# Performance work log

Measured on AMD Instinct MI355X. Metric: run time of the kernel, lower is better.

Reference implementation:

```python
import jax, jax.numpy as jnp
import numpy as np

EPS = 1e-8
TAU = 1.0


def _spatial_adjacency(segments, n_seg):
    # segments: (B, H, W) int. Counts 4-neighbour pixel adjacencies between segments;
    # diagonal counts pixels per segment (self loops kept).
    B, H, W = segments.shape
    b = jnp.arange(B)[:, None]
    adj = jnp.zeros((B, n_seg, n_seg), jnp.float32)
    flat = segments.reshape(B, -1)
    adj = adj.at[b, flat, flat].add(1.0)  # self loops = segment sizes
    s1 = segments[:, :, :-1].reshape(B, -1)
    s2 = segments[:, :, 1:].reshape(B, -1)
    adj = adj.at[b, s1, s2].add(1.0).at[b, s2, s1].add(1.0)
    v1 = segments[:, :-1, :].reshape(B, -1)
    v2 = segments[:, 1:, :].reshape(B, -1)
    adj = adj.at[b, v1, v2].add(1.0).at[b, v2, v1].add(1.0)
    return adj


def _proximity_adjacency(segments, n_seg):
    adj = _spatial_adjacency(segments, n_seg)
    # zero connections of node 0 except its diagonal
    adj = adj.at[:, 1:, 0].set(0.0).at[:, 0, 1:].set(0.0)
    size_node = jnp.diagonal(adj, axis1=-2, axis2=-1)
    new_diag = adj.sum(axis=2) - size_node + 1.0
    idx = jnp.arange(n_seg)
    adj = adj.at[:, idx, idx].set(new_diag)
    # normalize_adjacency(binarize=True, normalize=False)
    return (adj > 0).astype(jnp.float32)


def setup_inputs() -> dict:
    key = jax.random.key(0)
    k1, k2, k3 = jax.random.split(key, 3)
    B, N, D, R = 8, 2048, 384, 64
    H = W = 256
    x = jax.random.normal(k1, (B, N, D), jnp.float32)
    segments = jax.random.randint(k2, (B, H, W), 0, N, jnp.int64)
    prototypes = jax.random.normal(k3, (1, R, D), jnp.float32)
    return {"x": x, "segments": segments, "prototypes": prototypes}


def reference(x, segments, prototypes):
    B, N, D = x.shape
    prox_adj = _proximity_adjacency(segments, N)  # (B, N, N) binary

    # node-presence mask (B, N)
    b = jnp.arange(B)[:, None]
    flat = segments.reshape(B, -1)
    mask = jnp.zeros((B, N), jnp.float32).at[b, flat].max(1.0)

    # cosine prototype clustering (Q = V = K = Identity)
    protos = prototypes[0]  # (R, D)
    qn = x / jnp.maximum(jnp.linalg.norm(x, axis=-1, keepdims=True), EPS)
    kn = protos / jnp.maximum(jnp.linalg.norm(protos, axis=-1, keepdims=True), EPS)
    Csim = (jnp.einsum('bnd,rd->bnr', qn, kn) + 1.0) * 0.5
    S = Csim / Csim.sum(axis=-1, keepdims=True)  # soft assignment (B, N, R)

    # cluster alignment loss (DEC-style sharpened-target KL, masked over present nodes)
    P = S ** 2 / (S.sum(axis=1, keepdims=True) + EPS)
    P = P / (P.sum(axis=-1, keepdims=True) + EPS)
    kl = (P * (jnp.log(P + EPS) - jnp.log(S + EPS))).sum(axis=-1)  # (B, N)
    loss = (kl * mask).sum() / (mask.sum() + EPS)

    # affinity adjacency from assignments
    C = jax.nn.softmax(S * TAU, axis=-1)  # (B, N, R)
    cn = jnp.linalg.norm(C, axis=-1)  # (B, N)
    proto_adj = jnp.einsum('bnr,bmr->bnm', C, C) / (cn[:, :, None] * cn[:, None, :] + EPS)
    adj = prox_adj * proto_adj
    # normalize_adjacency(normalize=True): row normalization
    adj = adj / (adj.sum(axis=-1, keepdims=True) + EPS)

    out = jnp.einsum('bnm,bmd->bnd', adj, x)  # adj @ values
    return out, segments, loss, C
```

## Files before the change

kernel.cpp:

```cpp
#include <hip/hip_runtime.h>
#include <hip/hip_bf16.h>

#define NB 8
#define NN 2048
#define ND 384
#define NR 64
#define OUT_ELEMS (NB*NN*ND)
#define SEG_ELEMS (NB*256*256)
#define NBLK_LOSS (NB*NN/4)

typedef float  f32x4  __attribute__((ext_vector_type(4)));
typedef short  bf16x8 __attribute__((ext_vector_type(8)));

__device__ inline float wsum(float v){
  #pragma unroll
  for(int o=32;o;o>>=1) v += __shfl_xor(v,o,64);
  return v;
}
__device__ inline float wmax(float v){
  #pragma unroll
  for(int o=32;o;o>>=1) v = fmaxf(v,__shfl_xor(v,o,64));
  return v;
}
__device__ inline unsigned short f2bf(float f){
  unsigned u = __float_as_uint(f);
  return (unsigned short)((u + 0x8000u) >> 16);
}

__device__ __forceinline__ void gl2lds16(const unsigned short* g, unsigned short* s){
  __builtin_amdgcn_global_load_lds(
      (const __attribute__((address_space(1))) unsigned int*)g,
      (__attribute__((address_space(3))) unsigned int*)s,
      16, 0, 0);
}

__global__ void k_proto(const float* __restrict__ protos, float* __restrict__ kn){
  int r = blockIdx.x, l = threadIdx.x;
  float v[6]; float ss = 0.f;
  #pragma unroll
  for(int i=0;i<6;i++){ v[i] = protos[r*ND + l*6 + i]; ss += v[i]*v[i]; }
  ss = wsum(ss);
  float inv = 1.f / fmaxf(sqrtf(ss), 1e-8f);
  #pragma unroll
  for(int i=0;i<6;i++) kn[r*ND + l*6 + i] = v[i]*inv;
}

__global__ __launch_bounds__(1024) void k_seg(const int* __restrict__ seg,
                                              float* __restrict__ mask,
                                              unsigned* __restrict__ prox){
  __shared__ unsigned lm[64*64];
  int tid = threadIdx.x;
  int b  = blockIdx.x & 7;
  int rg = blockIdx.x >> 3;
  int base = rg << 6;
  for(int i=tid; i<64*64; i+=1024) lm[i] = 0u;
  __syncthreads();
  const int* sb = seg + b*65536;

#define PAIR(S, S2) { \
    if((S) != (S2) && (S) != 0 && (S2) != 0){ \
      if(((S )>>6)==rg) atomicOr(&lm[(((S )&63)<<6) + ((S2)>>5)], 1u<<((S2)&31)); \
      if(((S2)>>6)==rg) atomicOr(&lm[(((S2)&63)<<6) + ((S )>>5)], 1u<<((S )&31)); \
    } }

  #pragma unroll 1
  for(int it=0; it<16; ++it){
    int g = it*1024 + tid;
    int p = g*4;
    int i = g >> 6;
    int j = (g & 63)*4;
    int4 a = *(const int4*)(sb + p);
    if((a.x>>6)==rg) mask[(b<<11) + a.x] = 1.f;
    if((a.y>>6)==rg) mask[(b<<11) + a.y] = 1.f;
    if((a.z>>6)==rg) mask[(b<<11) + a.z] = 1.f;
    if((a.w>>6)==rg) mask[(b<<11) + a.w] = 1.f;
    PAIR(a.x, a.y); PAIR(a.y, a.z); PAIR(a.z, a.w);
    if(j < 252){
      int n = sb[p + 4];
      PAIR(a.w, n);
    }
    if(i < 255){
      int4 v = *(const int4*)(sb + p + 256);
      PAIR(a.x, v.x); PAIR(a.y, v.y); PAIR(a.z, v.z); PAIR(a.w, v.w);
    }
  }
#undef PAIR
  __syncthreads();
  unsigned* dst = prox + ((size_t)(b<<11) + base)*64;
  *(uint4*)(dst + tid*4) = *(const uint4*)&lm[tid*4];
}

__global__ __launch_bounds__(256) void k_csim(const float* __restrict__ x,
                                              const float* __restrict__ kn,
                                              float* __restrict__ Sout,
                                              unsigned short* __restrict__ xTbf,
                                              float* __restrict__ part){
  __shared__ float xT[32*68];
  __shared__ float kT[32*68];
  __shared__ float xinvS[64];
  __shared__ float csh[16*64];
  int t = threadIdx.x;
  int m0 = blockIdx.x * 64;
  float acc[4][4] = {};
  int mload = t>>2, koff = (t&3)*8;
  int mb = (t>>4)*4, rb = (t&15)*4;
  float ssq = 0.f;
  for(int c=0;c<12;c++){
    int k0 = c*32;
    __syncthreads();
    const float4* xg = (const float4*)(x + (size_t)(m0+mload)*ND + k0 + koff);
    float4 a = xg[0], bq = xg[1];
    ssq += a.x*a.x + a.y*a.y + a.z*a.z + a.w*a.w
         + bq.x*bq.x + bq.y*bq.y + bq.z*bq.z + bq.w*bq.w;
    xT[(koff+0)*68+mload]=a.x;  xT[(koff+1)*68+mload]=a.y;  xT[(koff+2)*68+mload]=a.z;  xT[(koff+3)*68+mload]=a.w;
    xT[(koff+4)*68+mload]=bq.x; xT[(koff+5)*68+mload]=bq.y; xT[(koff+6)*68+mload]=bq.z; xT[(koff+7)*68+mload]=bq.w;
    const float4* kg = (const float4*)(kn + mload*ND + k0 + koff);
    float4 ka = kg[0], kb = kg[1];
    kT[(koff+0)*68+mload]=ka.x; kT[(koff+1)*68+mload]=ka.y; kT[(koff+2)*68+mload]=ka.z; kT[(koff+3)*68+mload]=ka.w;
    kT[(koff+4)*68+mload]=kb.x; kT[(koff+5)*68+mload]=kb.y; kT[(koff+6)*68+mload]=kb.z; kT[(koff+7)*68+mload]=kb.w;
    __syncthreads();
    {
      int k2 = t>>3, mo = (t&7)*8;
      const float* src = &xT[k2*68 + mo];
      float4 aa = *(const float4*)src;
      float4 bb = *(const float4*)(src+4);
      uint4 o;
      o.x = (unsigned)f2bf(aa.x) | ((unsigned)f2bf(aa.y)<<16);
      o.y = (unsigned)f2bf(aa.z) | ((unsigned)f2bf(aa.w)<<16);
      o.z = (unsigned)f2bf(bb.x) | ((unsigned)f2bf(bb.y)<<16);
      o.w = (unsigned)f2bf(bb.z) | ((unsigned)f2bf(bb.w)<<16);
      int bb2 = m0 >> 11, ml = m0 & 2047;
      *(uint4*)(xTbf + ((size_t)(bb2*ND + k0 + k2))*NN + ml + mo) = o;
    }
    for(int k=0;k<32;k++){
      float xv[4], kv[4];
      *(float4*)xv = *(const float4*)&xT[k*68+mb];
      *(float4*)kv = *(const float4*)&kT[k*68+rb];
      #pragma unroll
      for(int mi=0;mi<4;mi++)
        #pragma unroll
        for(int ri=0;ri<4;ri++) acc[mi][ri] += xv[mi]*kv[ri];
    }
  }
  ssq += __shfl_xor(ssq,1,64);
  ssq += __shfl_xor(ssq,2,64);
  if((t&3)==0) xinvS[mload] = 1.f / fmaxf(sqrtf(ssq), 1e-8f);
  __syncthreads();
  float sv[4][4];
  #pragma unroll
  for(int mi=0;mi<4;mi++){
    float xin = xinvS[mb+mi];
    float rsum = 0.f;
    #pragma unroll
    for(int ri=0;ri<4;ri++){
      float vv = (acc[mi][ri]*xin + 1.f)*0.5f;
      sv[mi][ri] = vv; rsum += vv;
    }
    rsum += __shfl_xor(rsum,1,64);
    rsum += __shfl_xor(rsum,2,64);
    rsum += __shfl_xor(rsum,4,64);
    rsum += __shfl_xor(rsum,8,64);
    float inv = 1.f/rsum;
    #pragma unroll
    for(int ri=0;ri<4;ri++) sv[mi][ri] *= inv;
    *(float4*)&Sout[(size_t)(m0+mb+mi)*NR + rb] = *(const float4*)sv[mi];
  }
  {
    float4 pc;
    pc.x = sv[0][0]+sv[1][0]+sv[2][0]+sv[3][0];
    pc.y = sv[0][1]+sv[1][1]+sv[2][1]+sv[3][1];
    pc.z = sv[0][2]+sv[1][2]+sv[2][2]+sv[3][2];
    pc.w = sv[0][3]+sv[1][3]+sv[2][3]+sv[3][3];
    *(float4*)&csh[(t>>4)*64 + rb] = pc;
  }
  __syncthreads();
  if(t < 64){
    float a = 0.f;
    #pragma unroll
    for(int g=0;g<16;g++) a += csh[g*64 + t];
    part[(size_t)blockIdx.x*64 + t] = a;
  }
}

__global__ void k_lossfc(float* Smat, const float* __restrict__ part,
                         const float* __restrict__ mask,
                         float* __restrict__ klp, float* __restrict__ mp,
                         unsigned short* __restrict__ Kbf){
  __shared__ float shk[4], shm[4];
  int w = threadIdx.x>>6, l = threadIdx.x&63;
  int node = blockIdx.x*4 + w;
  int b = node >> 11;
  float s = Smat[(size_t)node*NR + l];
  float csm = 0.f;
  #pragma unroll
  for(int c=0;c<32;c++) csm += part[(size_t)((b<<5)+c)*64 + l];
  float p = s*s/(csm + 1e-8f);
  float ps = wsum(p);
  float P = p/(ps + 1e-8f);
  float term = P*(logf(P + 1e-8f) - logf(s + 1e-8f));
  float kl = wsum(term);
  if(l==0){ float mv = mask[node]; shk[w] = kl*mv; shm[w] = mv; }
  float mx = wmax(s);
  float e = expf(s - mx);
  float Z = wsum(e);
  float c = e / Z;
  float cn2 = wsum(c*c);
  Smat[(size_t)node*NR + l] = c;
  Kbf[(size_t)node*NR + l] = f2bf(c * rsqrtf(cn2));
  __syncthreads();
  if(threadIdx.x==0){
    klp[blockIdx.x] = shk[0]+shk[1]+shk[2]+shk[3];
    mp [blockIdx.x] = shm[0]+shm[1]+shm[2]+shm[3];
  }
}

__global__ __launch_bounds__(256) void k_qk(const unsigned short* __restrict__ Kbf,
                                            const unsigned* __restrict__ prox,
                                            unsigned short* __restrict__ Pbf){
  __shared__ short Plds[64*72];
  int tid = threadIdx.x;
  int w = tid>>6, l = tid&63, q = l>>4, li = l&15;
  int b  = blockIdx.x & 7;
  int qt = (blockIdx.x>>3) & 31;
  int kt = blockIdx.x >> 8;
  const unsigned short* Kb = Kbf + (size_t)b*NN*NR;

  int arow = qt*64 + w*16 + li;
  bf16x8 af[2];
  af[0] = *(const bf16x8*)(Kb + (size_t)arow*NR + q*8);
  af[1] = *(const bf16x8*)(Kb + (size_t)arow*NR + 32 + q*8);
  f32x4 pacc[4] = {(f32x4)(0.f),(f32x4)(0.f),(f32x4)(0.f),(f32x4)(0.f)};
  #pragma unroll
  for(int f=0;f<4;f++){
    int brow = kt*64 + f*16 + li;
    bf16x8 b0 = *(const bf16x8*)(Kb + (size_t)brow*NR + q*8);
    bf16x8 b1 = *(const bf16x8*)(Kb + (size_t)brow*NR + 32 + q*8);
    pacc[f] = __builtin_amdgcn_mfma_f32_16x16x32_bf16(af[0], b0, pacc[f], 0,0,0);
    pacc[f] = __builtin_amdgcn_mfma_f32_16x16x32_bf16(af[1], b1, pacc[f], 0,0,0);
  }
  #pragma unroll
  for(int r=0;r<4;r++){
    int lrow = w*16 + q*4 + r;
    int grow = qt*64 + lrow;
    uint2 mw = *(const uint2*)(prox + ((size_t)(b*NN + grow))*64 + kt*2);
    if(qt==kt){
      if((lrow>>5)==0) mw.x |= 1u<<(lrow&31); else mw.y |= 1u<<(lrow&31);
    }
    #pragma unroll
    for(int f=0;f<4;f++){
      unsigned wd = (f<2) ? mw.x : mw.y;
      float v = ((wd >> ((f&1)*16 + li)) & 1u) ? pacc[f][r] : 0.f;
      Plds[lrow*72 + f*16 + li] = (short)f2bf(v);
    }
  }
  __syncthreads();
  {
    int row = tid>>2, sg = tid&3;
    const uint4* src = (const uint4*)&Plds[row*72 + sg*16];
    unsigned short* dst = Pbf + ((size_t)(b*NN + qt*64 + row))*NN + kt*64 + sg*16;
    uint4 v0 = src[0], v1 = *(const uint4*)((const short*)src + 8);
    *(uint4*)dst = v0;
    *(uint4*)(dst + 8) = v1;
  }
}

__global__ __launch_bounds__(256, 3) void k_pv(const unsigned short* __restrict__ Pbf,
                                               const unsigned short* __restrict__ xTbf,
                                               float* __restrict__ out){
  __shared__ unsigned short Al[64*32];
  __shared__ unsigned short Bl[128*32];
  int tid = threadIdx.x;
  int w = tid>>6, l = tid&63, q = l>>4, li = l&15;
  int b  = blockIdx.x & 7;
  int mt = (blockIdx.x>>3) & 31;
  int ct = blockIdx.x >> 8;
  int m0 = mt*64;
  int d0 = ct*128;
  const unsigned short* Pb  = Pbf  + (size_t)b*NN*NN;
  const unsigned short* xTb = xTbf + (size_t)b*ND*NN;

  int wr = w & 1, wc = w >> 1;

  int lr = l>>2, lk = (l&3)*8;
  const unsigned short* gsrc0; const unsigned short* gsrc1; const unsigned short* gsrc2;
  unsigned short* ldst0; unsigned short* ldst1; unsigned short* ldst2;
  {
    int id0 = w*3, id1 = w*3+1, id2 = w*3+2;
    ldst0 = (id0<4 ? Al + id0*512 : Bl + (id0-4)*512);
    ldst1 = (id1<4 ? Al + id1*512 : Bl + (id1-4)*512);
    ldst2 = (id2<4 ? Al + id2*512 : Bl + (id2-4)*512);
    gsrc0 = (id0<4 ? Pb + (size_t)(m0 + id0*16 + lr)*NN + lk
                   : xTb + (size_t)(d0 + (id0-4)*16 + lr)*NN + lk);
    gsrc1 = (id1<4 ? Pb + (size_t)(m0 + id1*16 + lr)*NN + lk
                   : xTb + (size_t)(d0 + (id1-4)*16 + lr)*NN + lk);
    gsrc2 = (id2<4 ? Pb + (size_t)(m0 + id2*16 + lr)*NN + lk
                   : xTb + (size_t)(d0 + (id2-4)*16 + lr)*NN + lk);
  }

  f32x4 acc[2][4];
  #pragma unroll
  for(int nc=0;nc<2;nc++)
    #pragma unroll
    for(int t=0;t<4;t++) acc[nc][t] = (f32x4)(0.f);
  f32x4 rs[2] = {(f32x4)(0.f),(f32x4)(0.f)};
  bf16x8 ones;
  #pragma unroll
  for(int i=0;i<8;i++) ones[i] = (short)0x3F80;

  for(int k0=0; k0<NN; k0+=32){
    __syncthreads();
    gl2lds16(gsrc0 + k0, ldst0);
    gl2lds16(gsrc1 + k0, ldst1);
    gl2lds16(gsrc2 + k0, ldst2);
    __syncthreads();
    bf16x8 a0 = *(const bf16x8*)&Al[(wr*32 +      li)*32 + q*8];
    bf16x8 a1 = *(const bf16x8*)&Al[(wr*32 + 16 + li)*32 + q*8];
    bf16x8 bv[4];
    #pragma unroll
    for(int t=0;t<4;t++)
      bv[t] = *(const bf16x8*)&Bl[(wc*64 + t*16 + li)*32 + q*8];
    #pragma unroll
    for(int t=0;t<4;t++){
      acc[0][t] = __builtin_amdgcn_mfma_f32_16x16x32_bf16(a0, bv[t], acc[0][t], 0,0,0);
      acc[1][t] = __builtin_amdgcn_mfma_f32_16x16x32_bf16(a1, bv[t], acc[1][t], 0,0,0);
    }
    rs[0] = __builtin_amdgcn_mfma_f32_16x16x32_bf16(a0, ones, rs[0], 0,0,0);
    rs[1] = __builtin_amdgcn_mfma_f32_16x16x32_bf16(a1, ones, rs[1], 0,0,0);
  }

  #pragma unroll
  for(int nc=0;nc<2;nc++)
    #pragma unroll
    for(int r=0;r<4;r++){
      int row = m0 + wr*32 + nc*16 + q*4 + r;
      float inv = 1.f/(rs[nc][r] + 1e-8f);
      float* orow = out + ((size_t)(b*NN + row))*ND + d0 + wc*64;
      #pragma unroll
      for(int t=0;t<4;t++)
        orow[t*16 + li] = acc[nc][t][r] * inv;
    }
}

__global__ void k_segout(const int* __restrict__ seg, float* __restrict__ o,
                         const float* __restrict__ klp, const float* __restrict__ mp,
                         float* __restrict__ outLoss){
  int tid = threadIdx.x;
  int i = blockIdx.x*256 + tid;
  o[i] = (float)seg[i];
  if(blockIdx.x==0){
    __shared__ float sa[4], sm[4];
    float a=0.f, m=0.f;
    for(int k=tid; k<NBLK_LOSS; k+=256){ a += klp[k]; m += mp[k]; }
    a = wsum(a); m = wsum(m);
    if((tid&63)==0){ sa[tid>>6]=a; sm[tid>>6]=m; }
    __syncthreads();
    if(tid==0)
      outLoss[0] = (sa[0]+sa[1]+sa[2]+sa[3])/((sm[0]+sm[1]+sm[2]+sm[3])+1e-8f);
  }
}

extern "C" void kernel_launch(void* const* d_in, const int* in_sizes, int n_in,
                              void* d_out, int out_size, void* d_ws, size_t ws_size,
                              hipStream_t stream) {
  const float* x      = (const float*)d_in[0];
  const int*   seg    = (const int*)d_in[1];
  const float* protos = (const float*)d_in[2];

  float* out     = (float*)d_out;
  float* outSeg  = out + OUT_ELEMS;
  float* outLoss = outSeg + SEG_ELEMS;
  float* outC    = outLoss + 1;

  unsigned short* xTbf = (unsigned short*)d_ws;
  unsigned short* Kbf  = xTbf + (size_t)NB*ND*NN;
  unsigned short* Pbf  = Kbf + (size_t)NB*NN*NR;
  float* kn      = (float*)(Pbf + (size_t)NB*NN*NN);
  float* maskp   = kn + NR*ND;
  unsigned* prox = (unsigned*)(maskp + NB*NN);
  float* part    = (float*)(prox + (size_t)NB*NN*64);
  float* klp     = part + NB*32*64;
  float* mp      = klp + NBLK_LOSS;

  hipMemsetAsync(maskp, 0, (size_t)NB*NN*4, stream);

  k_proto <<<dim3(NR),           dim3(64),   0, stream>>>(protos, kn);
  k_seg   <<<dim3(256),          dim3(1024), 0, stream>>>(seg, maskp, prox);
  k_csim  <<<dim3(NB*NN/64),     dim3(256),  0, stream>>>(x, kn, outC, xTbf, part);
  k_lossfc<<<dim3(NBLK_LOSS),    dim3(256),  0, stream>>>(outC, part, maskp, klp, mp, Kbf);
  k_qk    <<<dim3(8192),         dim3(256),  0, stream>>>(Kbf, prox, Pbf);
  k_pv    <<<dim3(768),          dim3(256),  0, stream>>>(Pbf, xTbf, out);
  k_segout<<<dim3(SEG_ELEMS/256),dim3(256),  0, stream>>>(seg, outSeg, klp, mp, outLoss);
}
```

Measured before the change: 231.1 us.

## Loop four key tiles per k_qk block with per-wave LDS staging, no block barrier

k_qk now processes four consecutive key tiles per block in a loop, reusing the A-fragment loads and cutting the grid from 8192 to 2048 blocks. Each wave stages its own 16 rows in a private LDS slice, so the block-wide __syncthreads is gone and each wave writes its own rows to Pbf. The aim is to reduce launch/block overhead and redundant A loads in exchange for less parallelism per launch. Writes and reads to a wave's LDS slice rely on intra-wave ordering without an explicit barrier.

```diff
diff --git a/kernel.cpp b/kernel.cpp
--- a/kernel.cpp
+++ b/kernel.cpp
@@ -217,47 +217,57 @@
 __global__ __launch_bounds__(256) void k_qk(const unsigned short* __restrict__ Kbf,
                                             const unsigned* __restrict__ prox,
                                             unsigned short* __restrict__ Pbf){
-  __shared__ short Plds[64*72];
+  __shared__ short Plds[4][16*72];
   int tid = threadIdx.x;
   int w = tid>>6, l = tid&63, q = l>>4, li = l&15;
   int b  = blockIdx.x & 7;
   int qt = (blockIdx.x>>3) & 31;
-  int kt = blockIdx.x >> 8;
+  int kc = blockIdx.x >> 8;
   const unsigned short* Kb = Kbf + (size_t)b*NN*NR;
+  short* myP = Plds[w];
 
   int arow = qt*64 + w*16 + li;
-  bf16x8 af[2];
-  af[0] = *(const bf16x8*)(Kb + (size_t)arow*NR + q*8);
-  af[1] = *(const bf16x8*)(Kb + (size_t)arow*NR + 32 + q*8);
-  f32x4 pacc[4] = {(f32x4)(0.f),(f32x4)(0.f),(f32x4)(0.f),(f32x4)(0.f)};
-  #pragma unroll
-  for(int f=0;f<4;f++){
-    int brow = kt*64 + f*16 + li;
-    bf16x8 b0 = *(const bf16x8*)(Kb + (size_t)brow*NR + q*8);
-    bf16x8 b1 = *(const bf16x8*)(Kb + (size_t)brow*NR + 32 + q*8);
-    pacc[f] = __builtin_amdgcn_mfma_f32_16x16x32_bf16(af[0], b0, pacc[f], 0,0,0);
-    pacc[f] = __builtin_amdgcn_mfma_f32_16x16x32_bf16(af[1], b1, pacc[f], 0,0,0);
-  }
-  #pragma unroll
-  for(int r=0;r<4;r++){
-    int lrow = w*16 + q*4 + r;
-    int grow = qt*64 + lrow;
-    uint2 mw = *(const uint2*)(prox + ((size_t)(b*NN + grow))*64 + kt*2);
-    if(qt==kt){
-      if((lrow>>5)==0) mw.x |= 1u<<(lrow&31); else mw.y |= 1u<<(lrow&31);
-    }
+  bf16x8 af0 = *(const bf16x8*)(Kb + (size_t)arow*NR + q*8);
+  bf16x8 af1 = *(const bf16x8*)(Kb + (size_t)arow*NR + 32 + q*8);
+
+  int srow = l>>2, sg = l&3;
+
+  #pragma unroll 1
+  for(int kt = kc*4; kt < kc*4 + 4; ++kt){
+    uint2 mw[4];
+    #pragma unroll
+    for(int r=0;r<4;r++)
+      mw[r] = *(const uint2*)(prox + ((size_t)(b*NN + qt*64 + w*16 + q*4 + r))*64 + kt*2);
+    bf16x8 b0[4], b1[4];
     #pragma unroll
     for(int f=0;f<4;f++){
-      unsigned wd = (f<2) ? mw.x : mw.y;
-      float v = ((wd >> ((f&1)*16 + li)) & 1u) ? pacc[f][r] : 0.f;
-      Plds[lrow*72 + f*16 + li] = (short)f2bf(v);
-    }
-  }
-  __syncthreads();
-  {
-    int row = tid>>2, sg = tid&3;
-    const uint4* src = (const uint4*)&Plds[row*72 + sg*16];
-    unsigned short* dst = Pbf + ((size_t)(b*NN + qt*64 + row))*NN + kt*64 + sg*16;
+      const unsigned short* p = Kb + (size_t)(kt*64 + f*16 + li)*NR + q*8;
+      b0[f] = *(const bf16x8*)p;
+      b1[f] = *(const bf16x8*)(p + 32);
+    }
+    f32x4 pacc[4] = {(f32x4)(0.f),(f32x4)(0.f),(f32x4)(0.f),(f32x4)(0.f)};
+    #pragma unroll
+    for(int f=0;f<4;f++){
+      pacc[f] = __builtin_amdgcn_mfma_f32_16x16x32_bf16(af0, b0[f], pacc[f], 0,0,0);
+      pacc[f] = __builtin_amdgcn_mfma_f32_16x16x32_bf16(af1, b1[f], pacc[f], 0,0,0);
+    }
+    #pragma unroll
+    for(int r=0;r<4;r++){
+      int lrow = q*4 + r;
+      int brow = w*16 + lrow;
+      uint2 m = mw[r];
+      if(qt==kt){
+        if((brow>>5)==0) m.x |= 1u<<(brow&31); else m.y |= 1u<<(brow&31);
+      }
+      #pragma unroll
+      for(int f=0;f<4;f++){
+        unsigned wd = (f<2) ? m.x : m.y;
+        float v = ((wd >> ((f&1)*16 + li)) & 1u) ? pacc[f][r] : 0.f;
+        myP[lrow*72 + f*16 + li] = (short)f2bf(v);
+      }
+    }
+    const uint4* src = (const uint4*)&myP[srow*72 + sg*16];
+    unsigned short* dst = Pbf + ((size_t)(b*NN + qt*64 + w*16 + srow))*NN + kt*64 + sg*16;
     uint4 v0 = src[0], v1 = *(const uint4*)((const short*)src + 8);
     *(uint4*)dst = v0;
     *(uint4*)(dst + 8) = v1;
@@ -387,7 +397,7 @@
   k_seg   <<<dim3(256),          dim3(1024), 0, stream>>>(seg, maskp, prox);
   k_csim  <<<dim3(NB*NN/64),     dim3(256),  0, stream>>>(x, kn, outC, xTbf, part);
   k_lossfc<<<dim3(NBLK_LOSS),    dim3(256),  0, stream>>>(outC, part, maskp, klp, mp, Kbf);
-  k_qk    <<<dim3(8192),         dim3(256),  0, stream>>>(Kbf, prox, Pbf);
+  k_qk    <<<dim3(2048),         dim3(256),  0, stream>>>(Kbf, prox, Pbf);
   k_pv    <<<dim3(768),          dim3(256),  0, stream>>>(Pbf, xTbf, out);
   k_segout<<<dim3(SEG_ELEMS/256),dim3(256),  0, stream>>>(seg, outSeg, klp, mp, outLoss);
 }
```

New measurement: 231.7 us. Within noise of the previous version (+0.3%).
